# Optimization experiments

Hardware: AMD Instinct MI355X
Metric: run time of the kernel (lower is better)

## Reference

```python
import jax, jax.numpy as jnp
import numpy as np

NUM_LEVELS = 4
CODES_PER_LEVEL = 1024
CODE_DIM = 256
BATCH = 65536


def setup_inputs() -> dict:
    key = jax.random.key(0)
    k_z, k_cb = jax.random.split(key)
    z = jax.random.normal(k_z, (BATCH, CODE_DIM), dtype=jnp.float32)
    # codebooks buffer: randn * code_dim**-0.5, matching torch init
    codebooks = jax.random.normal(k_cb, (NUM_LEVELS, CODES_PER_LEVEL, CODE_DIM), dtype=jnp.float32) * (CODE_DIM ** -0.5)
    return {"z": z, "codebooks": codebooks}


def _quantize(z, codebooks):
    """Sequential residual VQ: per level, squared-dist argmin + gather.
    z: [B, D]; codebooks: [L, K, D]. Returns z_q [B, D], codes [B, L] int32.
    """
    residual = z
    z_q = jnp.zeros_like(z)
    codes_list = []
    for lvl in range(codebooks.shape[0]):  # small fixed loop over levels
        cb = codebooks[lvl]  # [K, D]
        # ||r - c||^2 = ||r||^2 - 2 r.c + ||c||^2  -> [B, K]
        dists = (jnp.sum(residual * residual, axis=-1, keepdims=True)
                 - 2.0 * jnp.einsum('bd,kd->bk', residual, cb)
                 + jnp.sum(cb * cb, axis=-1))
        codes_lvl = jnp.argmin(dists, axis=1)  # [B]
        selected = cb[codes_lvl]               # gather [B, D]
        z_q = z_q + selected
        residual = residual - selected
        codes_list.append(codes_lvl)
    codes = jnp.stack(codes_list, axis=1)  # [B, L]
    return z_q, codes


def reference(z, codebooks):
    z_q, codes = _quantize(z, codebooks)
    # straight-through: gradient flows to z only
    z_q_st = z + jax.lax.stop_gradient(z_q - z)
    commit_loss = jnp.mean(jnp.square(jax.lax.stop_gradient(z_q) - z))
    return z_q_st, codes, commit_loss
```

## Files before the change

kernel.cpp:

```cpp
#include <hip/hip_runtime.h>


#define NB 65536
#define ND 256
#define NK 1024
#define NL 4
#define MROWS 128
#define NBLK (NB / MROWS)
#define CHUNK 64
#define NCH (NK / CHUNK)
#define BSTR 264
#define FLAG_MARGIN 1e-3f

typedef __attribute__((ext_vector_type(8))) short short8;
typedef __attribute__((ext_vector_type(4))) float f32x4;

__device__ inline unsigned short f2bf(float x) {
  unsigned u = __float_as_uint(x);
  u = u + 0x7FFFu + ((u >> 16) & 1u);
  return (unsigned short)(u >> 16);
}
__device__ inline float bf2f(unsigned short h) {
  return __uint_as_float(((unsigned)h) << 16);
}

__device__ float np_sum256_sq(const float* __restrict__ a) {
#pragma clang fp contract(off)
  float out[2];
  for (int h = 0; h < 2; ++h) {
    const float* p = a + 128 * h;
    float r[8];
    for (int j = 0; j < 8; ++j) r[j] = p[j] * p[j];
    for (int i = 8; i < 128; i += 8)
      for (int j = 0; j < 8; ++j) r[j] += p[i + j] * p[i + j];
    out[h] = ((r[0] + r[1]) + (r[2] + r[3])) + ((r[4] + r[5]) + (r[6] + r[7]));
  }
  return out[0] + out[1];
}
__device__ float np_einsum256(const float* __restrict__ r,
                              const float* __restrict__ c) {
#pragma clang fp contract(off)
  float e[4] = {0.f, 0.f, 0.f, 0.f};
  for (int d = 0; d < 256; d += 4) {
    e[0] += r[d + 0] * c[d + 0];
    e[1] += r[d + 1] * c[d + 1];
    e[2] += r[d + 2] * c[d + 2];
    e[3] += r[d + 3] * c[d + 3];
  }
  return (e[0] + e[1]) + (e[2] + e[3]);
}
__device__ float np_dist(const float* __restrict__ resrow,
                         const float* __restrict__ crow, float r2) {
#pragma clang fp contract(off)
  float E = np_einsum256(resrow, crow);
  float c2 = np_sum256_sq(crow);
  float t1 = r2 - 2.0f * E;
  return t1 + c2;
}

__global__ void prep_split(const float* __restrict__ cb,
                           unsigned short* __restrict__ whi,
                           unsigned short* __restrict__ wlo) {
  int i = blockIdx.x * 256 + threadIdx.x;
  float c = cb[i];
  unsigned short h = f2bf(c);
  whi[i] = h;
  wlo[i] = f2bf(c - bf2f(h));
}
__global__ void prep_c2(const float* __restrict__ cb, float* __restrict__ c2) {
  int k = blockIdx.x;
  int lane = threadIdx.x;
  const float* p = cb + (size_t)k * ND + lane * 4;
  double s = (double)p[0]*p[0] + (double)p[1]*p[1]
           + (double)p[2]*p[2] + (double)p[3]*p[3];
  for (int off = 32; off >= 1; off >>= 1) s += __shfl_down(s, off);
  if (lane == 0) c2[k] = (float)s;
}


__global__ __launch_bounds__(256, 2)
void rvq_main(const float* __restrict__ z, const float* __restrict__ cbf,
              const unsigned short* __restrict__ whi,
              const unsigned short* __restrict__ wlo,
              const float* __restrict__ c2w, float* __restrict__ out) {
  extern __shared__ char smem[];
  unsigned short* bhi = (unsigned short*)smem;
  unsigned short* blo = bhi + 64 * BSTR;
  float* c2s  = (float*)(smem + 67584);
  int*   selh = (int*)(smem + 71680);
  int*   flags= (int*)(smem + 73728);
  float* mscr = (float*)smem;
  float* resr = (float*)(smem + 32768);
  float* redf = (float*)(smem + 34816);
  int*   redk = (int*)(smem + 35840);
  double* lred= (double*)smem;

  const int tid  = threadIdx.x;
  const int wave = tid >> 6, lane = tid & 63;
  const int quad = lane >> 4, lx = lane & 15;
  const int blk  = blockIdx.x;

  for (int lvl = 0; lvl < NL; ++lvl) {
    __syncthreads();
#pragma unroll
    for (int t = 0; t < 4; ++t)
      c2s[t * 256 + tid] = c2w[lvl * NK + t * 256 + tid];

    short8 Ah[2][8], Al[2][8];
#pragma unroll
    for (int s = 0; s < 2; ++s) {
      const int rloc = wave * 32 + s * 16 + lx;
      const size_t rg = (size_t)(blk * MROWS + rloc);
#pragma unroll
      for (int ks = 0; ks < 8; ++ks) {
        const int k0 = 32 * ks + quad * 8;
        const float* zp = z + rg * ND + k0;
        float4 p0 = *(const float4*)zp;
        float4 p1 = *(const float4*)(zp + 4);
        for (int l = 0; l < lvl; ++l) {
          int sel = selh[rloc * 4 + l];
          const float* cp = cbf + (size_t)(l * NK + sel) * ND + k0;
          float4 q0 = *(const float4*)cp, q1 = *(const float4*)(cp + 4);
          p0.x -= q0.x; p0.y -= q0.y; p0.z -= q0.z; p0.w -= q0.w;
          p1.x -= q1.x; p1.y -= q1.y; p1.z -= q1.z; p1.w -= q1.w;
        }
        float v0[8] = {p0.x, p0.y, p0.z, p0.w, p1.x, p1.y, p1.z, p1.w};
#pragma unroll
        for (int j = 0; j < 8; ++j) {
          unsigned short h = f2bf(v0[j]);
          Ah[s][ks][j] = (short)h;
          Al[s][ks][j] = (short)f2bf(v0[j] - bf2f(h));
        }
      }
    }

    float m1[8], m2[8]; int i1[8];
#pragma unroll
    for (int t = 0; t < 8; ++t) { m1[t] = 1e30f; m2[t] = 1e30f; i1[t] = 0; }

#pragma unroll 1
    for (int ch = 0; ch < NCH; ++ch) {
      __syncthreads();
      {
        const size_t gb = (size_t)lvl * NK * ND + (size_t)ch * CHUNK * ND;
#pragma unroll
        for (int it = 0; it < 8; ++it) {
          int i = it * 256 + tid;
          int code = i >> 5, col = i & 31;
          uint4 vh = *(const uint4*)(whi + gb + (size_t)code * ND + col * 8);
          *(uint4*)(bhi + code * BSTR + col * 8) = vh;
          uint4 vl = *(const uint4*)(wlo + gb + (size_t)code * ND + col * 8);
          *(uint4*)(blo + code * BSTR + col * 8) = vl;
        }
      }
      __syncthreads();
#pragma unroll 1
      for (int tile = 0; tile < 4; ++tile) {
        f32x4 a0a = {0,0,0,0}, a0b = {0,0,0,0}, a1a = {0,0,0,0}, a1b = {0,0,0,0};
        const int crow = tile * 16 + lx;
        const unsigned short* bph = bhi + crow * BSTR + quad * 8;
        const unsigned short* bpl = blo + crow * BSTR + quad * 8;
#pragma unroll
        for (int ks = 0; ks < 8; ks += 2) {
          short8 vb0 = *(const short8*)(bph + 32 * ks);
          short8 wb0 = *(const short8*)(bpl + 32 * ks);
          short8 vb1 = *(const short8*)(bph + 32 * ks + 32);
          short8 wb1 = *(const short8*)(bpl + 32 * ks + 32);
          a0a = __builtin_amdgcn_mfma_f32_16x16x32_bf16(Ah[0][ks], vb0, a0a, 0, 0, 0);
          a1a = __builtin_amdgcn_mfma_f32_16x16x32_bf16(Ah[1][ks], vb0, a1a, 0, 0, 0);
          a0a = __builtin_amdgcn_mfma_f32_16x16x32_bf16(Al[0][ks], vb0, a0a, 0, 0, 0);
          a1a = __builtin_amdgcn_mfma_f32_16x16x32_bf16(Al[1][ks], vb0, a1a, 0, 0, 0);
          a0a = __builtin_amdgcn_mfma_f32_16x16x32_bf16(Ah[0][ks], wb0, a0a, 0, 0, 0);
          a1a = __builtin_amdgcn_mfma_f32_16x16x32_bf16(Ah[1][ks], wb0, a1a, 0, 0, 0);
          a0b = __builtin_amdgcn_mfma_f32_16x16x32_bf16(Ah[0][ks + 1], vb1, a0b, 0, 0, 0);
          a1b = __builtin_amdgcn_mfma_f32_16x16x32_bf16(Ah[1][ks + 1], vb1, a1b, 0, 0, 0);
          a0b = __builtin_amdgcn_mfma_f32_16x16x32_bf16(Al[0][ks + 1], vb1, a0b, 0, 0, 0);
          a1b = __builtin_amdgcn_mfma_f32_16x16x32_bf16(Al[1][ks + 1], vb1, a1b, 0, 0, 0);
          a0b = __builtin_amdgcn_mfma_f32_16x16x32_bf16(Ah[0][ks + 1], wb1, a0b, 0, 0, 0);
          a1b = __builtin_amdgcn_mfma_f32_16x16x32_bf16(Ah[1][ks + 1], wb1, a1b, 0, 0, 0);
        }
        const int kidx = ch * CHUNK + crow;
        const float c2v = c2s[kidx];
#pragma unroll
        for (int s = 0; s < 2; ++s)
#pragma unroll
          for (int r = 0; r < 4; ++r) {
            float e = (s == 0) ? (a0a[r] + a0b[r]) : (a1a[r] + a1b[r]);
            float d = fmaf(-2.0f, e, c2v);
            int st = s * 4 + r;
            if (d < m1[st]) { m2[st] = m1[st]; m1[st] = d; i1[st] = kidx; }
            else if (d < m2[st]) m2[st] = d;
          }
      }
    }

    __syncthreads();
#pragma unroll
    for (int t = 0; t < 8; ++t) {
      int rloc = wave * 32 + (t >> 2) * 16 + quad * 4 + (t & 3);
      float* p = mscr + (rloc * 16 + lx) * 4;
      p[0] = m1[t]; p[1] = m2[t]; p[2] = __int_as_float(i1[t]);
    }
    __syncthreads();
    if (tid < MROWS) {
      float gm1 = 1e30f, gm2 = 1e30f; int gi1 = 0x7fffffff;
      for (int t = 0; t < 16; ++t) {
        const float* p = mscr + (tid * 16 + t) * 4;
        float a1 = p[0], a2 = p[1]; int ai = __float_as_int(p[2]);
        if (a1 < gm1 || (a1 == gm1 && ai < gi1)) {
          gm2 = fminf(gm1, a2); gm1 = a1; gi1 = ai;
        } else {
          gm2 = fminf(gm2, a1);
        }
      }
      selh[tid * 4 + lvl] = gi1;
      flags[tid] = (gm2 - gm1 <= FLAG_MARGIN) ? 1 : 0;
    }
    __syncthreads();

    for (int r = 0; r < MROWS; ++r) {
      if (flags[r]) {
        {
          float v = z[(size_t)(blk * MROWS + r) * ND + tid];
          for (int l = 0; l < lvl; ++l)
            v -= cbf[(size_t)(l * NK + selh[r * 4 + l]) * ND + tid];
          resr[tid] = v;
        }
        __syncthreads();
        float r2 = np_sum256_sq(resr);
        float bd = 1e30f; int bk = 0x7fffffff;
        for (int u = 0; u < 4; ++u) {
          int k = u * 256 + tid;
          float dd = np_dist(resr, cbf + (size_t)(lvl * NK + k) * ND, r2);
          if (dd < bd || (dd == bd && k < bk)) { bd = dd; bk = k; }
        }
        redf[tid] = bd; redk[tid] = bk;
        __syncthreads();
        if (tid == 0) {
          float gb = 1e30f; int gk = 0x7fffffff;
          for (int t2 = 0; t2 < 256; ++t2) {
            if (redf[t2] < gb || (redf[t2] == gb && redk[t2] < gk)) {
              gb = redf[t2]; gk = redk[t2];
            }
          }
          selh[r * 4 + lvl] = gk;
        }
        __syncthreads();
      }
    }
  }

  __syncthreads();
  double lacc = 0.0;
#pragma unroll 1
  for (int it = 0; it < 32; ++it) {
    int i = it * 256 + tid;
    int row = i >> 6, dc = i & 63;
    size_t rg = (size_t)(blk * MROWS + row);
    float4 z4 = *(const float4*)(z + rg * ND + dc * 4);
    float4 q; q.x = 0.f; q.y = 0.f; q.z = 0.f; q.w = 0.f;
    for (int l = 0; l < NL; ++l) {
      int sel = selh[row * 4 + l];
      float4 c4 = *(const float4*)(cbf + (size_t)(l * NK + sel) * ND + dc * 4);
      q.x += c4.x; q.y += c4.y; q.z += c4.z; q.w += c4.w;
    }
    *(float4*)(out + rg * ND + dc * 4) = q;
    float dx = q.x - z4.x, dy = q.y - z4.y, dz = q.z - z4.z, dw = q.w - z4.w;
    lacc += (double)dx * dx + (double)dy * dy + (double)dz * dz + (double)dw * dw;
  }
  if (tid < MROWS) {
    for (int l = 0; l < NL; ++l)
      out[(size_t)NB * ND + (size_t)(blk * MROWS + tid) * NL + l] =
          (float)selh[tid * 4 + l];
  }
  __syncthreads();
  lred[tid] = lacc;
  __syncthreads();
  if (tid == 0) {
    double s = 0.0;
    for (int t = 0; t < 256; ++t) s += lred[t];
    atomicAdd(out + (size_t)NB * ND + (size_t)NB * NL,
              (float)(s / ((double)NB * (double)ND)));
  }
}

extern "C" void kernel_launch(void* const* d_in, const int* in_sizes, int n_in,
                              void* d_out, int out_size, void* d_ws, size_t ws_size,
                              hipStream_t stream) {
  const float* z  = (const float*)d_in[0];
  const float* cb = (const float*)d_in[1];
  float* out = (float*)d_out;

  unsigned short* whi = (unsigned short*)d_ws;
  unsigned short* wlo = whi + (size_t)NL * NK * ND;
  float* c2w = (float*)(wlo + (size_t)NL * NK * ND);

  hipMemsetAsync((void*)(out + (size_t)NB * ND + (size_t)NB * NL), 0,
                 sizeof(float), stream);

  prep_split<<<dim3(4096), dim3(256), 0, stream>>>(cb, whi, wlo);
  prep_c2<<<dim3(4096), dim3(64), 0, stream>>>(cb, c2w);

  const size_t shmem = 74240;
  hipFuncSetAttribute((const void*)rvq_main,
                      hipFuncAttributeMaxDynamicSharedMemorySize, (int)shmem);
  rvq_main<<<dim3(NBLK), dim3(256), shmem, stream>>>(z, cb, whi, wlo, c2w, out);
}
```

Baseline: 1.250 ms.

## Double-buffer codebook chunks with async global-to-LDS loads and XOR swizzle

```diff
diff --git a/kernel.cpp b/kernel.cpp
--- a/kernel.cpp
+++ b/kernel.cpp
@@ -7,13 +7,16 @@
 #define NL 4
 #define MROWS 128
 #define NBLK (NB / MROWS)
-#define CHUNK 64
+#define CHUNK 32
 #define NCH (NK / CHUNK)
-#define BSTR 264
 #define FLAG_MARGIN 1e-3f
 
 typedef __attribute__((ext_vector_type(8))) short short8;
 typedef __attribute__((ext_vector_type(4))) float f32x4;
+typedef const __attribute__((address_space(1))) unsigned int gu32;
+typedef __attribute__((address_space(3))) unsigned int lu32;
+
+#define MFMA __builtin_amdgcn_mfma_f32_16x16x32_bf16
 
 __device__ inline unsigned short f2bf(float x) {
   unsigned u = __float_as_uint(x);
@@ -78,21 +81,40 @@
 }
 
 
+__device__ __forceinline__ void stage_chunk(
+    const unsigned short* __restrict__ whi,
+    const unsigned short* __restrict__ wlo,
+    unsigned short* buf, int lvl, int ch, int wave, int lane) {
+  const int rp = lane >> 5;
+  const int scol = lane & 31;
+#pragma unroll
+  for (int j = 0; j < 8; ++j) {
+    const int g = wave * 8 + j;
+    const int region = g >> 4;
+    const int gi = g & 15;
+    const int row = gi * 2 + rp;
+    const int gcol = scol ^ (row & 7);
+    const unsigned short* src = (region ? wlo : whi)
+        + (size_t)lvl * NK * ND + (size_t)(ch * CHUNK + row) * ND + gcol * 8;
+    char* dst = (char*)buf + region * 16384 + gi * 1024;
+    __builtin_amdgcn_global_load_lds((gu32*)src, (lu32*)dst, 16, 0, 0);
+  }
+}
+
 __global__ __launch_bounds__(256, 2)
 void rvq_main(const float* __restrict__ z, const float* __restrict__ cbf,
               const unsigned short* __restrict__ whi,
               const unsigned short* __restrict__ wlo,
               const float* __restrict__ c2w, float* __restrict__ out) {
   extern __shared__ char smem[];
-  unsigned short* bhi = (unsigned short*)smem;
-  unsigned short* blo = bhi + 64 * BSTR;
-  float* c2s  = (float*)(smem + 67584);
-  int*   selh = (int*)(smem + 71680);
-  int*   flags= (int*)(smem + 73728);
-  float* mscr = (float*)smem;
-  float* resr = (float*)(smem + 32768);
-  float* redf = (float*)(smem + 34816);
-  int*   redk = (int*)(smem + 35840);
+  unsigned short* bufA = (unsigned short*)smem;
+  unsigned short* bufB = (unsigned short*)(smem + 32768);
+  float* c2s  = (float*)(smem + 65536);
+  int*   selh = (int*)(smem + 69632);
+  int*   flags= (int*)(smem + 71680);
+  float* resr = (float*)smem;
+  float* redf = (float*)(smem + 1024);
+  int*   redk = (int*)(smem + 2048);
   double* lred= (double*)smem;
 
   const int tid  = threadIdx.x;
@@ -138,47 +160,46 @@
 #pragma unroll
     for (int t = 0; t < 8; ++t) { m1[t] = 1e30f; m2[t] = 1e30f; i1[t] = 0; }
 
+    __syncthreads();
+    stage_chunk(whi, wlo, bufA, lvl, 0, wave, lane);
+    stage_chunk(whi, wlo, bufB, lvl, 1, wave, lane);
+
 #pragma unroll 1
     for (int ch = 0; ch < NCH; ++ch) {
-      __syncthreads();
-      {
-        const size_t gb = (size_t)lvl * NK * ND + (size_t)ch * CHUNK * ND;
-#pragma unroll
-        for (int it = 0; it < 8; ++it) {
-          int i = it * 256 + tid;
-          int code = i >> 5, col = i & 31;
-          uint4 vh = *(const uint4*)(whi + gb + (size_t)code * ND + col * 8);
-          *(uint4*)(bhi + code * BSTR + col * 8) = vh;
-          uint4 vl = *(const uint4*)(wlo + gb + (size_t)code * ND + col * 8);
-          *(uint4*)(blo + code * BSTR + col * 8) = vl;
-        }
-      }
-      __syncthreads();
+      if (ch + 1 < NCH) asm volatile("s_waitcnt vmcnt(8)" ::: "memory");
+      else              asm volatile("s_waitcnt vmcnt(0)" ::: "memory");
+      __builtin_amdgcn_s_barrier();
+      __builtin_amdgcn_sched_barrier(0);
+      const unsigned short* bh = (ch & 1) ? bufB : bufA;
 #pragma unroll 1
-      for (int tile = 0; tile < 4; ++tile) {
+      for (int tile = 0; tile < 2; ++tile) {
         f32x4 a0a = {0,0,0,0}, a0b = {0,0,0,0}, a1a = {0,0,0,0}, a1b = {0,0,0,0};
         const int crow = tile * 16 + lx;
-        const unsigned short* bph = bhi + crow * BSTR + quad * 8;
-        const unsigned short* bpl = blo + crow * BSTR + quad * 8;
+        const unsigned short* bp = bh + crow * 256;
+        const int xr = lx & 7;
+        __builtin_amdgcn_s_setprio(1);
 #pragma unroll
         for (int ks = 0; ks < 8; ks += 2) {
-          short8 vb0 = *(const short8*)(bph + 32 * ks);
-          short8 wb0 = *(const short8*)(bpl + 32 * ks);
-          short8 vb1 = *(const short8*)(bph + 32 * ks + 32);
-          short8 wb1 = *(const short8*)(bpl + 32 * ks + 32);
-          a0a = __builtin_amdgcn_mfma_f32_16x16x32_bf16(Ah[0][ks], vb0, a0a, 0, 0, 0);
-          a1a = __builtin_amdgcn_mfma_f32_16x16x32_bf16(Ah[1][ks], vb0, a1a, 0, 0, 0);
-          a0a = __builtin_amdgcn_mfma_f32_16x16x32_bf16(Al[0][ks], vb0, a0a, 0, 0, 0);
-          a1a = __builtin_amdgcn_mfma_f32_16x16x32_bf16(Al[1][ks], vb0, a1a, 0, 0, 0);
-          a0a = __builtin_amdgcn_mfma_f32_16x16x32_bf16(Ah[0][ks], wb0, a0a, 0, 0, 0);
-          a1a = __builtin_amdgcn_mfma_f32_16x16x32_bf16(Ah[1][ks], wb0, a1a, 0, 0, 0);
-          a0b = __builtin_amdgcn_mfma_f32_16x16x32_bf16(Ah[0][ks + 1], vb1, a0b, 0, 0, 0);
-          a1b = __builtin_amdgcn_mfma_f32_16x16x32_bf16(Ah[1][ks + 1], vb1, a1b, 0, 0, 0);
-          a0b = __builtin_amdgcn_mfma_f32_16x16x32_bf16(Al[0][ks + 1], vb1, a0b, 0, 0, 0);
-          a1b = __builtin_amdgcn_mfma_f32_16x16x32_bf16(Al[1][ks + 1], vb1, a1b, 0, 0, 0);
-          a0b = __builtin_amdgcn_mfma_f32_16x16x32_bf16(Ah[0][ks + 1], wb1, a0b, 0, 0, 0);
-          a1b = __builtin_amdgcn_mfma_f32_16x16x32_bf16(Ah[1][ks + 1], wb1, a1b, 0, 0, 0);
-        }
+          const int s0 = ((ks * 4 + quad) ^ xr) * 8;
+          const int s1 = ((ks * 4 + 4 + quad) ^ xr) * 8;
+          short8 vb0 = *(const short8*)(bp + s0);
+          short8 wb0 = *(const short8*)(bp + 8192 + s0);
+          short8 vb1 = *(const short8*)(bp + s1);
+          short8 wb1 = *(const short8*)(bp + 8192 + s1);
+          a0a = MFMA(Ah[0][ks], vb0, a0a, 0, 0, 0);
+          a1a = MFMA(Ah[1][ks], vb0, a1a, 0, 0, 0);
+          a0a = MFMA(Al[0][ks], vb0, a0a, 0, 0, 0);
+          a1a = MFMA(Al[1][ks], vb0, a1a, 0, 0, 0);
+          a0a = MFMA(Ah[0][ks], wb0, a0a, 0, 0, 0);
+          a1a = MFMA(Ah[1][ks], wb0, a1a, 0, 0, 0);
+          a0b = MFMA(Ah[0][ks + 1], vb1, a0b, 0, 0, 0);
+          a1b = MFMA(Ah[1][ks + 1], vb1, a1b, 0, 0, 0);
+          a0b = MFMA(Al[0][ks + 1], vb1, a0b, 0, 0, 0);
+          a1b = MFMA(Al[1][ks + 1], vb1, a1b, 0, 0, 0);
+          a0b = MFMA(Ah[0][ks + 1], wb1, a0b, 0, 0, 0);
+          a1b = MFMA(Ah[1][ks + 1], wb1, a1b, 0, 0, 0);
+        }
+        __builtin_amdgcn_s_setprio(0);
         const int kidx = ch * CHUNK + crow;
         const float c2v = c2s[kidx];
 #pragma unroll
@@ -192,60 +213,68 @@
             else if (d < m2[st]) m2[st] = d;
           }
       }
-    }
-
-    __syncthreads();
+      asm volatile("s_waitcnt lgkmcnt(0)" ::: "memory");
+      __builtin_amdgcn_s_barrier();
+      __builtin_amdgcn_sched_barrier(0);
+      if (ch + 2 < NCH)
+        stage_chunk(whi, wlo, (ch & 1) ? bufB : bufA, lvl, ch + 2, wave, lane);
+    }
+
+    int myflag = 0;
 #pragma unroll
     for (int t = 0; t < 8; ++t) {
-      int rloc = wave * 32 + (t >> 2) * 16 + quad * 4 + (t & 3);
-      float* p = mscr + (rloc * 16 + lx) * 4;
-      p[0] = m1[t]; p[1] = m2[t]; p[2] = __int_as_float(i1[t]);
-    }
-    __syncthreads();
-    if (tid < MROWS) {
-      float gm1 = 1e30f, gm2 = 1e30f; int gi1 = 0x7fffffff;
-      for (int t = 0; t < 16; ++t) {
-        const float* p = mscr + (tid * 16 + t) * 4;
-        float a1 = p[0], a2 = p[1]; int ai = __float_as_int(p[2]);
-        if (a1 < gm1 || (a1 == gm1 && ai < gi1)) {
-          gm2 = fminf(gm1, a2); gm1 = a1; gi1 = ai;
+      float a1 = m1[t], a2 = m2[t]; int ai = i1[t];
+#pragma unroll
+      for (int off = 1; off < 16; off <<= 1) {
+        float o1 = __shfl_xor(a1, off);
+        float o2 = __shfl_xor(a2, off);
+        int   oi = __shfl_xor(ai, off);
+        if (o1 < a1 || (o1 == a1 && oi < ai)) {
+          a2 = fminf(a1, o2); a1 = o1; ai = oi;
         } else {
-          gm2 = fminf(gm2, a1);
-        }
-      }
-      selh[tid * 4 + lvl] = gi1;
-      flags[tid] = (gm2 - gm1 <= FLAG_MARGIN) ? 1 : 0;
-    }
-    __syncthreads();
-
-    for (int r = 0; r < MROWS; ++r) {
-      if (flags[r]) {
-        {
-          float v = z[(size_t)(blk * MROWS + r) * ND + tid];
-          for (int l = 0; l < lvl; ++l)
-            v -= cbf[(size_t)(l * NK + selh[r * 4 + l]) * ND + tid];
-          resr[tid] = v;
-        }
-        __syncthreads();
-        float r2 = np_sum256_sq(resr);
-        float bd = 1e30f; int bk = 0x7fffffff;
-        for (int u = 0; u < 4; ++u) {
-          int k = u * 256 + tid;
-          float dd = np_dist(resr, cbf + (size_t)(lvl * NK + k) * ND, r2);
-          if (dd < bd || (dd == bd && k < bk)) { bd = dd; bk = k; }
-        }
-        redf[tid] = bd; redk[tid] = bk;
-        __syncthreads();
-        if (tid == 0) {
-          float gb = 1e30f; int gk = 0x7fffffff;
-          for (int t2 = 0; t2 < 256; ++t2) {
-            if (redf[t2] < gb || (redf[t2] == gb && redk[t2] < gk)) {
-              gb = redf[t2]; gk = redk[t2];
+          a2 = fminf(a2, o1);
+        }
+      }
+      if (lx == 0) {
+        int rloc = wave * 32 + (t >> 2) * 16 + quad * 4 + (t & 3);
+        selh[rloc * 4 + lvl] = ai;
+        int f = (a2 - a1 <= FLAG_MARGIN) ? 1 : 0;
+        flags[rloc] = f;
+        myflag |= f;
+      }
+    }
+    int anyf = __syncthreads_or(myflag);
+
+    if (anyf) {
+      for (int r = 0; r < MROWS; ++r) {
+        if (flags[r]) {
+          {
+            float v = z[(size_t)(blk * MROWS + r) * ND + tid];
+            for (int l = 0; l < lvl; ++l)
+              v -= cbf[(size_t)(l * NK + selh[r * 4 + l]) * ND + tid];
+            resr[tid] = v;
+          }
+          __syncthreads();
+          float r2 = np_sum256_sq(resr);
+          float bd = 1e30f; int bk = 0x7fffffff;
+          for (int u = 0; u < 4; ++u) {
+            int k = u * 256 + tid;
+            float dd = np_dist(resr, cbf + (size_t)(lvl * NK + k) * ND, r2);
+            if (dd < bd || (dd == bd && k < bk)) { bd = dd; bk = k; }
+          }
+          redf[tid] = bd; redk[tid] = bk;
+          __syncthreads();
+          if (tid == 0) {
+            float gb = 1e30f; int gk = 0x7fffffff;
+            for (int t2 = 0; t2 < 256; ++t2) {
+              if (redf[t2] < gb || (redf[t2] == gb && redk[t2] < gk)) {
+                gb = redf[t2]; gk = redk[t2];
+              }
             }
+            selh[r * 4 + lvl] = gk;
           }
-          selh[r * 4 + lvl] = gk;
-        }
-        __syncthreads();
+          __syncthreads();
+        }
       }
     }
   }
@@ -301,7 +330,7 @@
   prep_split<<<dim3(4096), dim3(256), 0, stream>>>(cb, whi, wlo);
   prep_c2<<<dim3(4096), dim3(64), 0, stream>>>(cb, c2w);
 
-  const size_t shmem = 74240;
+  const size_t shmem = 72192;
   hipFuncSetAttribute((const void*)rvq_main,
                       hipFuncAttributeMaxDynamicSharedMemorySize, (int)shmem);
   rvq_main<<<dim3(NBLK), dim3(256), shmem, stream>>>(z, cb, whi, wlo, c2w, out);
```

New measurement: 1.135 ms. -9.2%, faster.
